# Performance work log

Hardware: AMD Instinct MI355X
Metric: run time of the kernel (lower is better)

The kernel has to match this reference:

```python
import jax, jax.numpy as jnp
import numpy as np

N, D_IN, D_OUT = 8192, 1024, 1024

def setup_inputs() -> dict:
    key = jax.random.key(0)
    kx, kq, kk, kv = jax.random.split(key, 4)
    # Linear weights stored as [in_dim, out_dim] (torch stores [out,in]; we pre-transpose)
    s = 1.0 / np.sqrt(D_IN)
    return {
        "x": jax.random.normal(kx, (N, D_IN), dtype=jnp.float32),
        "Wq": jax.random.uniform(kq, (D_IN, D_OUT), dtype=jnp.float32, minval=-s, maxval=s),
        "Wk": jax.random.uniform(kk, (D_IN, D_OUT), dtype=jnp.float32, minval=-s, maxval=s),
        "Wv": jax.random.uniform(kv, (D_IN, D_OUT), dtype=jnp.float32, minval=-s, maxval=s),
    }

def reference(x, Wq, Wk, Wv):
    # Faithful to source: query_w = keys_L(x), key_w = queries_L(x) -- a name swap
    # that is just a relabeling of independent random weights. The earlier
    # parameter matmuls in the source are dead code (overwritten) and omitted.
    q = x @ Wk          # [N, D_OUT]
    k = x @ Wq          # [N, D_OUT]
    v = x @ Wv          # [N, D_OUT]
    scores = (q @ k.T) / jnp.sqrt(jnp.asarray(D_OUT, dtype=q.dtype))  # [N, N]
    weights = jax.nn.softmax(scores, axis=-1)
    return weights @ v  # [N, D_OUT]
```

## Files before the change

kernel.cpp:

```cpp
#include <hip/hip_runtime.h>
#include <hip/hip_bf16.h>
#include <stdint.h>

typedef __bf16 v8bf __attribute__((ext_vector_type(8)));
typedef __bf16 v4bf __attribute__((ext_vector_type(4)));
typedef float  v4f  __attribute__((ext_vector_type(4)));

#define AS1 __attribute__((address_space(1)))
#define AS3 __attribute__((address_space(3)))

__device__ __forceinline__ void load16_lds(const void* g, void* l) {
  __builtin_amdgcn_global_load_lds((const AS1 uint32_t*)g, (AS3 uint32_t*)l, 16, 0, 0);
}

__global__ __launch_bounds__(256) void k_cvt_x(const float* __restrict__ x,
                                               __bf16* __restrict__ xb) {
  size_t i = ((size_t)blockIdx.x * 256 + threadIdx.x) * 4;
  float4 f = *(const float4*)(x + i);
  v4bf b; b[0] = (__bf16)f.x; b[1] = (__bf16)f.y; b[2] = (__bf16)f.z; b[3] = (__bf16)f.w;
  *(v4bf*)(xb + i) = b;
}

__global__ __launch_bounds__(256) void k_wtrans(const float* __restrict__ W,
                                                __bf16* __restrict__ Wt) {
  __shared__ float tile[64][65];
  int r0 = blockIdx.x * 64, c0 = blockIdx.y * 64;
  int t = threadIdx.x;
  #pragma unroll
  for (int p = 0; p < 16; p++) {
    int idx = p * 256 + t; int rr = idx >> 6, cc = idx & 63;
    tile[rr][cc] = W[(size_t)(r0 + rr) * 1024 + c0 + cc];
  }
  __syncthreads();
  #pragma unroll
  for (int p = 0; p < 16; p++) {
    int idx = p * 256 + t; int rr = idx >> 6, cc = idx & 63;
    Wt[(size_t)(c0 + rr) * 1024 + r0 + cc] = (__bf16)tile[cc][rr];
  }
}

__global__ __launch_bounds__(256) void k_vtrans(const __bf16* __restrict__ V,
                                                __bf16* __restrict__ Vt) {
  __shared__ __bf16 tile[64][66];
  int r0 = blockIdx.x * 64, c0 = blockIdx.y * 64;
  int t = threadIdx.x;
  #pragma unroll
  for (int p = 0; p < 16; p++) {
    int idx = p * 256 + t; int rr = idx >> 6, cc = idx & 63;
    tile[rr][cc] = V[(size_t)(r0 + rr) * 1024 + c0 + cc];
  }
  __syncthreads();
  #pragma unroll
  for (int p = 0; p < 16; p++) {
    int idx = p * 256 + t; int rr = idx >> 6, cc = idx & 63;
    Vt[(size_t)(c0 + rr) * 8192 + r0 + cc] = tile[cc][rr];
  }
}

__global__ __launch_bounds__(256) void k_zero(float* __restrict__ p) {
  size_t i = ((size_t)blockIdx.x * 256 + threadIdx.x) * 4;
  *(float4*)(p + i) = make_float4(0.f, 0.f, 0.f, 0.f);
}

__global__ __launch_bounds__(256) void k_rowinv(const float* __restrict__ rs,
                                                float* __restrict__ ri) {
  int i = blockIdx.x * 256 + threadIdx.x;
  ri[i] = 1.0f / rs[i];
}

template <int EPI>
__global__ __launch_bounds__(256, 2) void gemm_nt(
    const __bf16* __restrict__ A, const __bf16* __restrict__ B,
    void* __restrict__ Cout, int M, int N, int K,
    __bf16* __restrict__ qp, __bf16* __restrict__ kp, __bf16* __restrict__ vp,
    float* __restrict__ rowsum, const float* __restrict__ rinv)
{
  __shared__ __bf16 Asm[128 * 32];
  __shared__ __bf16 Bsm[128 * 32];
  const int tid = threadIdx.x;
  const int wave = tid >> 6, lane = tid & 63;
  const size_t m0 = (size_t)blockIdx.x * 128;
  const size_t n0 = (size_t)blockIdx.y * 128;
  const int wm = (wave >> 1) * 64, wn = (wave & 1) * 64;

  v4f acc[4][4];
  #pragma unroll
  for (int i = 0; i < 4; i++)
    #pragma unroll
    for (int j = 0; j < 4; j++) acc[i][j] = (v4f)0.f;

  const int lr = lane >> 2;
  const int lc = (lane & 3) * 8;
  const int fr = lane & 15;
  const int fk = (lane >> 4) * 8;
  const size_t sK = (size_t)K;

  for (int k0 = 0; k0 < K; k0 += 32) {
    #pragma unroll
    for (int i = 0; i < 2; i++) {
      const int seg = i * 4 + wave;
      const int row = seg * 16 + lr;
      load16_lds(A + (m0 + row) * sK + (size_t)(k0 + lc), Asm + seg * 512);
      load16_lds(B + (n0 + row) * sK + (size_t)(k0 + lc), Bsm + seg * 512);
    }
    __syncthreads();
    v8bf a_frag[4], b_frag[4];
    #pragma unroll
    for (int i = 0; i < 4; i++)
      a_frag[i] = *(const v8bf*)(Asm + (wm + i * 16 + fr) * 32 + fk);
    #pragma unroll
    for (int j = 0; j < 4; j++)
      b_frag[j] = *(const v8bf*)(Bsm + (wn + j * 16 + fr) * 32 + fk);
    #pragma unroll
    for (int i = 0; i < 4; i++)
      #pragma unroll
      for (int j = 0; j < 4; j++)
        acc[i][j] = __builtin_amdgcn_mfma_f32_16x16x32_bf16(a_frag[i], b_frag[j], acc[i][j], 0, 0, 0);
    __syncthreads();
  }

  const int er = (lane >> 4) * 4;
  const int ec = lane & 15;

  if (EPI == 3) {
    float rpart[4][4];
    #pragma unroll
    for (int i = 0; i < 4; i++)
      #pragma unroll
      for (int r = 0; r < 4; r++) rpart[i][r] = 0.f;
    #pragma unroll
    for (int i = 0; i < 4; i++)
      #pragma unroll
      for (int j = 0; j < 4; j++) {
        const size_t col = n0 + wn + j * 16 + ec;
        #pragma unroll
        for (int r = 0; r < 4; r++) {
          const size_t rowg = m0 + wm + i * 16 + er + r;
          float e = __expf(acc[i][j][r]);
          ((__bf16*)Cout)[rowg * (size_t)N + col] = (__bf16)e;
          rpart[i][r] += e;
        }
      }
    #pragma unroll
    for (int i = 0; i < 4; i++)
      #pragma unroll
      for (int r = 0; r < 4; r++) {
        float s = rpart[i][r];
        s += __shfl_xor(s, 1); s += __shfl_xor(s, 2);
        s += __shfl_xor(s, 4); s += __shfl_xor(s, 8);
        if (ec == 0) atomicAdd(&rowsum[m0 + wm + i * 16 + er + r], s);
      }
    return;
  }

  #pragma unroll
  for (int i = 0; i < 4; i++)
    #pragma unroll
    for (int j = 0; j < 4; j++) {
      const size_t col = n0 + wn + j * 16 + ec;
      #pragma unroll
      for (int r = 0; r < 4; r++) {
        const size_t rowg = m0 + wm + i * 16 + er + r;
        float val = acc[i][j][r];
        if (EPI == 0) {
          ((float*)Cout)[rowg * (size_t)N + col] = val * rinv[rowg];
        } else {
          const int buf = (int)(col >> 10);
          const size_t cc = col & 1023;
          __bf16* dst = (buf == 0) ? qp : ((buf == 1) ? kp : vp);
          if (buf == 0) val *= 0.03125f;
          dst[rowg * 1024 + cc] = (__bf16)val;
        }
      }
    }
}

extern "C" void kernel_launch(void* const* d_in, const int* in_sizes, int n_in,
                              void* d_out, int out_size, void* d_ws, size_t ws_size,
                              hipStream_t stream) {
  const float* x  = (const float*)d_in[0];
  const float* Wq = (const float*)d_in[1];
  const float* Wk = (const float*)d_in[2];
  const float* Wv = (const float*)d_in[3];
  float* out = (float*)d_out;

  const size_t N = 8192, D = 1024;
  char* ws = (char*)d_ws;
  size_t off = 0;
  __bf16* xb = (__bf16*)(ws + off); off += N * D * 2;
  __bf16* wt = (__bf16*)(ws + off); off += 3 * D * D * 2;
  __bf16* q  = (__bf16*)(ws + off); off += N * D * 2;
  __bf16* k  = (__bf16*)(ws + off); off += N * D * 2;
  __bf16* v  = (__bf16*)(ws + off); off += N * D * 2;
  __bf16* vt = (__bf16*)(ws + off); off += N * D * 2;
  __bf16* S  = (__bf16*)(ws + off); off += N * N * 2;
  float* rowsum = (float*)(ws + off); off += N * 4;
  float* rinv   = (float*)(ws + off); off += N * 4;
  if (ws_size < off) return;

  k_cvt_x<<<dim3(8192), dim3(256), 0, stream>>>(x, xb);
  k_wtrans<<<dim3(16, 16), dim3(256), 0, stream>>>(Wk, wt);
  k_wtrans<<<dim3(16, 16), dim3(256), 0, stream>>>(Wq, wt + D * D);
  k_wtrans<<<dim3(16, 16), dim3(256), 0, stream>>>(Wv, wt + 2 * D * D);
  k_zero<<<dim3(8), dim3(256), 0, stream>>>(rowsum);
  gemm_nt<2><<<dim3(64, 24), dim3(256), 0, stream>>>(xb, wt, nullptr, 8192, 3072, 1024, q, k, v, nullptr, nullptr);
  k_vtrans<<<dim3(128, 16), dim3(256), 0, stream>>>(v, vt);
  gemm_nt<3><<<dim3(64, 64), dim3(256), 0, stream>>>(q, k, S, 8192, 8192, 1024, nullptr, nullptr, nullptr, rowsum, nullptr);
  k_rowinv<<<dim3(32), dim3(256), 0, stream>>>(rowsum, rinv);
  gemm_nt<0><<<dim3(64, 8), dim3(256), 0, stream>>>(S, vt, out, 8192, 1024, 8192, nullptr, nullptr, nullptr, nullptr, rinv);
}
```

Baseline: 500.6 us.

## Load GEMM fragments directly from global into registers with double buffering

The GEMM drops the LDS staging and both __syncthreads per k-step. Each wave now loads its MFMA fragments straight from global memory into registers, keeping two 32-wide k slices in flight so loads overlap the MFMAs. Launch bounds rise to 3 blocks per CU. The cost is that tiles are no longer shared across waves through LDS, so A and B are each fetched twice from global/L2 per block, and the loads are strided 16-byte row accesses that coalesce poorly.

Measured after the change: 1.189 ms. +137.6%, slower.

```diff
diff --git a/kernel.cpp b/kernel.cpp
--- a/kernel.cpp
+++ b/kernel.cpp
@@ -5,13 +5,6 @@
 typedef __bf16 v8bf __attribute__((ext_vector_type(8)));
 typedef __bf16 v4bf __attribute__((ext_vector_type(4)));
 typedef float  v4f  __attribute__((ext_vector_type(4)));
-
-#define AS1 __attribute__((address_space(1)))
-#define AS3 __attribute__((address_space(3)))
-
-__device__ __forceinline__ void load16_lds(const void* g, void* l) {
-  __builtin_amdgcn_global_load_lds((const AS1 uint32_t*)g, (AS3 uint32_t*)l, 16, 0, 0);
-}
 
 __global__ __launch_bounds__(256) void k_cvt_x(const float* __restrict__ x,
                                                __bf16* __restrict__ xb) {
@@ -69,55 +62,76 @@
 }
 
 template <int EPI>
-__global__ __launch_bounds__(256, 2) void gemm_nt(
+__global__ __launch_bounds__(256, 3) void gemm_nt(
     const __bf16* __restrict__ A, const __bf16* __restrict__ B,
     void* __restrict__ Cout, int M, int N, int K,
     __bf16* __restrict__ qp, __bf16* __restrict__ kp, __bf16* __restrict__ vp,
     float* __restrict__ rowsum, const float* __restrict__ rinv)
 {
-  __shared__ __bf16 Asm[128 * 32];
-  __shared__ __bf16 Bsm[128 * 32];
   const int tid = threadIdx.x;
   const int wave = tid >> 6, lane = tid & 63;
   const size_t m0 = (size_t)blockIdx.x * 128;
   const size_t n0 = (size_t)blockIdx.y * 128;
   const int wm = (wave >> 1) * 64, wn = (wave & 1) * 64;
-
-  v4f acc[4][4];
-  #pragma unroll
-  for (int i = 0; i < 4; i++)
-    #pragma unroll
-    for (int j = 0; j < 4; j++) acc[i][j] = (v4f)0.f;
-
-  const int lr = lane >> 2;
-  const int lc = (lane & 3) * 8;
   const int fr = lane & 15;
   const int fk = (lane >> 4) * 8;
   const size_t sK = (size_t)K;
-
-  for (int k0 = 0; k0 < K; k0 += 32) {
-    #pragma unroll
-    for (int i = 0; i < 2; i++) {
-      const int seg = i * 4 + wave;
-      const int row = seg * 16 + lr;
-      load16_lds(A + (m0 + row) * sK + (size_t)(k0 + lc), Asm + seg * 512);
-      load16_lds(B + (n0 + row) * sK + (size_t)(k0 + lc), Bsm + seg * 512);
+  const size_t rstep = 16 * sK;
+
+  const __bf16* Ab = A + (m0 + wm + fr) * sK + fk;
+  const __bf16* Bb = B + (n0 + wn + fr) * sK + fk;
+
+  v4f acc[4][4];
+  #pragma unroll
+  for (int i = 0; i < 4; i++)
+    #pragma unroll
+    for (int j = 0; j < 4; j++) acc[i][j] = (v4f)0.f;
+
+  v8bf a0[4], b0[4], a1[4], b1[4];
+  #pragma unroll
+  for (int i = 0; i < 4; i++) {
+    a0[i] = *(const v8bf*)(Ab + (size_t)i * rstep);
+    b0[i] = *(const v8bf*)(Bb + (size_t)i * rstep);
+  }
+  #pragma unroll
+  for (int i = 0; i < 4; i++) {
+    a1[i] = *(const v8bf*)(Ab + (size_t)i * rstep + 32);
+    b1[i] = *(const v8bf*)(Bb + (size_t)i * rstep + 32);
+  }
+
+  int k0 = 0;
+  for (; k0 + 64 < K; k0 += 64) {
+    #pragma unroll
+    for (int i = 0; i < 4; i++)
+      #pragma unroll
+      for (int j = 0; j < 4; j++)
+        acc[i][j] = __builtin_amdgcn_mfma_f32_16x16x32_bf16(a0[i], b0[j], acc[i][j], 0, 0, 0);
+    #pragma unroll
+    for (int i = 0; i < 4; i++) {
+      a0[i] = *(const v8bf*)(Ab + (size_t)i * rstep + (size_t)(k0 + 64));
+      b0[i] = *(const v8bf*)(Bb + (size_t)i * rstep + (size_t)(k0 + 64));
     }
-    __syncthreads();
-    v8bf a_frag[4], b_frag[4];
-    #pragma unroll
-    for (int i = 0; i < 4; i++)
-      a_frag[i] = *(const v8bf*)(Asm + (wm + i * 16 + fr) * 32 + fk);
+    #pragma unroll
+    for (int i = 0; i < 4; i++)
+      #pragma unroll
+      for (int j = 0; j < 4; j++)
+        acc[i][j] = __builtin_amdgcn_mfma_f32_16x16x32_bf16(a1[i], b1[j], acc[i][j], 0, 0, 0);
+    #pragma unroll
+    for (int i = 0; i < 4; i++) {
+      a1[i] = *(const v8bf*)(Ab + (size_t)i * rstep + (size_t)(k0 + 96));
+      b1[i] = *(const v8bf*)(Bb + (size_t)i * rstep + (size_t)(k0 + 96));
+    }
+  }
+  #pragma unroll
+  for (int i = 0; i < 4; i++)
     #pragma unroll
     for (int j = 0; j < 4; j++)
-      b_frag[j] = *(const v8bf*)(Bsm + (wn + j * 16 + fr) * 32 + fk);
-    #pragma unroll
-    for (int i = 0; i < 4; i++)
-      #pragma unroll
-      for (int j = 0; j < 4; j++)
-        acc[i][j] = __builtin_amdgcn_mfma_f32_16x16x32_bf16(a_frag[i], b_frag[j], acc[i][j], 0, 0, 0);
-    __syncthreads();
-  }
+      acc[i][j] = __builtin_amdgcn_mfma_f32_16x16x32_bf16(a0[i], b0[j], acc[i][j], 0, 0, 0);
+  #pragma unroll
+  for (int i = 0; i < 4; i++)
+    #pragma unroll
+    for (int j = 0; j < 4; j++)
+      acc[i][j] = __builtin_amdgcn_mfma_f32_16x16x32_bf16(a1[i], b1[j], acc[i][j], 0, 0, 0);
 
   const int er = (lane >> 4) * 4;
   const int ec = lane & 15;
```

## Double-buffer GEMM LDS tiles with XOR swizzle and merge weight transposes

Applied to the files above, without the earlier changes.

The bf16 NT GEMM now uses two LDS buffers. It prefetches the next K-slice through global_load_lds while MFMAs run on the current one, which drops one barrier per iteration. The LDS layout gets an XOR swizzle on the 16-byte chunks so fragment reads avoid bank conflicts. Launch bounds rise from 2 to 5 blocks per CU to push occupancy, which caps registers and risks spilling the 64-float accumulator tile. The three weight-transpose launches become one launch using a z-grid.

New measurement: 863.1 us. 72.4% more time.

```diff
diff --git a/kernel.cpp b/kernel.cpp
--- a/kernel.cpp
+++ b/kernel.cpp
@@ -21,9 +21,13 @@
   *(v4bf*)(xb + i) = b;
 }
 
-__global__ __launch_bounds__(256) void k_wtrans(const float* __restrict__ W,
-                                                __bf16* __restrict__ Wt) {
+__global__ __launch_bounds__(256) void k_wtrans3(const float* __restrict__ W0,
+                                                 const float* __restrict__ W1,
+                                                 const float* __restrict__ W2,
+                                                 __bf16* __restrict__ Wt) {
   __shared__ float tile[64][65];
+  const float* W = (blockIdx.z == 0) ? W0 : ((blockIdx.z == 1) ? W1 : W2);
+  __bf16* dst = Wt + (size_t)blockIdx.z * 1024 * 1024;
   int r0 = blockIdx.x * 64, c0 = blockIdx.y * 64;
   int t = threadIdx.x;
   #pragma unroll
@@ -35,7 +39,7 @@
   #pragma unroll
   for (int p = 0; p < 16; p++) {
     int idx = p * 256 + t; int rr = idx >> 6, cc = idx & 63;
-    Wt[(size_t)(c0 + rr) * 1024 + r0 + cc] = (__bf16)tile[cc][rr];
+    dst[(size_t)(c0 + rr) * 1024 + r0 + cc] = (__bf16)tile[cc][rr];
   }
 }
 
@@ -69,14 +73,14 @@
 }
 
 template <int EPI>
-__global__ __launch_bounds__(256, 2) void gemm_nt(
+__global__ __launch_bounds__(256, 5) void gemm_nt(
     const __bf16* __restrict__ A, const __bf16* __restrict__ B,
     void* __restrict__ Cout, int M, int N, int K,
     __bf16* __restrict__ qp, __bf16* __restrict__ kp, __bf16* __restrict__ vp,
     float* __restrict__ rowsum, const float* __restrict__ rinv)
 {
-  __shared__ __bf16 Asm[128 * 32];
-  __shared__ __bf16 Bsm[128 * 32];
+  __shared__ __bf16 Asm[2][128 * 32];
+  __shared__ __bf16 Bsm[2][128 * 32];
   const int tid = threadIdx.x;
   const int wave = tid >> 6, lane = tid & 63;
   const size_t m0 = (size_t)blockIdx.x * 128;
@@ -89,28 +93,45 @@
     #pragma unroll
     for (int j = 0; j < 4; j++) acc[i][j] = (v4f)0.f;
 
-  const int lr = lane >> 2;
-  const int lc = (lane & 3) * 8;
+  const int srow   = lane >> 2;
+  const int schunk = (lane & 3) ^ (srow & 3);
   const int fr = lane & 15;
-  const int fk = (lane >> 4) * 8;
+  const int hi = lane >> 4;
+  const int slot = hi ^ (fr & 3);
   const size_t sK = (size_t)K;
 
-  for (int k0 = 0; k0 < K; k0 += 32) {
-    #pragma unroll
-    for (int i = 0; i < 2; i++) {
-      const int seg = i * 4 + wave;
-      const int row = seg * 16 + lr;
-      load16_lds(A + (m0 + row) * sK + (size_t)(k0 + lc), Asm + seg * 512);
-      load16_lds(B + (n0 + row) * sK + (size_t)(k0 + lc), Bsm + seg * 512);
+  const __bf16* Ag = A + m0 * sK;
+  const __bf16* Bg = B + n0 * sK;
+
+  #pragma unroll
+  for (int p = 0; p < 2; p++) {
+    const int seg = wave * 2 + p;
+    const size_t row = (size_t)(seg * 16 + srow);
+    load16_lds(Ag + row * sK + schunk * 8, &Asm[0][seg * 512]);
+    load16_lds(Bg + row * sK + schunk * 8, &Bsm[0][seg * 512]);
+  }
+  __syncthreads();
+
+  int buf = 0;
+  for (int k0 = 0; k0 < K; k0 += 32, buf ^= 1) {
+    if (k0 + 32 < K) {
+      #pragma unroll
+      for (int p = 0; p < 2; p++) {
+        const int seg = wave * 2 + p;
+        const size_t row = (size_t)(seg * 16 + srow);
+        load16_lds(Ag + row * sK + (size_t)(k0 + 32) + schunk * 8, &Asm[buf ^ 1][seg * 512]);
+        load16_lds(Bg + row * sK + (size_t)(k0 + 32) + schunk * 8, &Bsm[buf ^ 1][seg * 512]);
+      }
     }
-    __syncthreads();
+    const __bf16* as = &Asm[buf][0];
+    const __bf16* bs = &Bsm[buf][0];
     v8bf a_frag[4], b_frag[4];
     #pragma unroll
     for (int i = 0; i < 4; i++)
-      a_frag[i] = *(const v8bf*)(Asm + (wm + i * 16 + fr) * 32 + fk);
+      a_frag[i] = *(const v8bf*)(as + (wm + i * 16 + fr) * 32 + slot * 8);
     #pragma unroll
     for (int j = 0; j < 4; j++)
-      b_frag[j] = *(const v8bf*)(Bsm + (wn + j * 16 + fr) * 32 + fk);
+      b_frag[j] = *(const v8bf*)(bs + (wn + j * 16 + fr) * 32 + slot * 8);
     #pragma unroll
     for (int i = 0; i < 4; i++)
       #pragma unroll
@@ -165,10 +186,10 @@
         if (EPI == 0) {
           ((float*)Cout)[rowg * (size_t)N + col] = val * rinv[rowg];
         } else {
-          const int buf = (int)(col >> 10);
+          const int b2 = (int)(col >> 10);
           const size_t cc = col & 1023;
-          __bf16* dst = (buf == 0) ? qp : ((buf == 1) ? kp : vp);
-          if (buf == 0) val *= 0.03125f;
+          __bf16* dst = (b2 == 0) ? qp : ((b2 == 1) ? kp : vp);
+          if (b2 == 0) val *= 0.03125f;
           dst[rowg * 1024 + cc] = (__bf16)val;
         }
       }
@@ -199,9 +220,7 @@
   if (ws_size < off) return;
 
   k_cvt_x<<<dim3(8192), dim3(256), 0, stream>>>(x, xb);
-  k_wtrans<<<dim3(16, 16), dim3(256), 0, stream>>>(Wk, wt);
-  k_wtrans<<<dim3(16, 16), dim3(256), 0, stream>>>(Wq, wt + D * D);
-  k_wtrans<<<dim3(16, 16), dim3(256), 0, stream>>>(Wv, wt + 2 * D * D);
+  k_wtrans3<<<dim3(16, 16, 3), dim3(256), 0, stream>>>(Wk, Wq, Wv, wt);
   k_zero<<<dim3(8), dim3(256), 0, stream>>>(rowsum);
   gemm_nt<2><<<dim3(64, 24), dim3(256), 0, stream>>>(xb, wt, nullptr, 8192, 3072, 1024, q, k, v, nullptr, nullptr);
   k_vtrans<<<dim3(128, 16), dim3(256), 0, stream>>>(v, vt);
```
